# Kernel tuning notes

Measured on AMD Instinct MI355X. Metric: run time of the kernel, lower is better.

## Reference

```python
import jax, jax.numpy as jnp
import numpy as np

EMBED = 256
HEADS = 8
LEVELS = 4
POINTS = 4
HEAD_DIM = EMBED // HEADS
SHAPES = np.array([[100, 134], [50, 67], [25, 34], [13, 17]], dtype=np.int64)  # (H, W) per level


def setup_inputs() -> dict:
    key = jax.random.key(0)
    ks = jax.random.split(key, 11)
    bs = 2
    nv = int(SHAPES.prod(axis=1).sum())  # 17821
    nq = nv
    s = 0.02
    return {
        "query": jax.random.normal(ks[0], (bs, nq, EMBED), jnp.float32),
        "reference_points": jax.random.uniform(ks[1], (bs, nq, LEVELS, 2), jnp.float32),
        "spatial_shapes": jnp.asarray(SHAPES),
        "Wv": jax.random.normal(ks[2], (EMBED, EMBED), jnp.float32) * s,
        "bv": jnp.zeros((EMBED,), jnp.float32),
        "Woff": jax.random.normal(ks[3], (HEADS * LEVELS * POINTS * 2, EMBED), jnp.float32) * s,
        "boff": jax.random.normal(ks[4], (HEADS * LEVELS * POINTS * 2,), jnp.float32) * s,
        "Wattn": jax.random.normal(ks[5], (HEADS * LEVELS * POINTS, EMBED), jnp.float32) * s,
        "battn": jnp.zeros((HEADS * LEVELS * POINTS,), jnp.float32),
        "Wout": jax.random.normal(ks[6], (EMBED, EMBED), jnp.float32) * s,
        "bout": jnp.zeros((EMBED,), jnp.float32),
    }


def _msda(value, shapes, loc, attn):
    # value: [bs, nv, heads, d]; loc: [bs, nq, heads, L, P, 2]; attn: [bs, nq, heads, L, P]
    bs, nq = loc.shape[0], loc.shape[1]
    out = jnp.zeros((bs, nq, HEADS, HEAD_DIM), value.dtype)
    bi = jnp.arange(bs)[:, None, None, None]
    hi = jnp.arange(HEADS)[None, None, :, None]
    start = 0
    for lvl in range(LEVELS):
        H, W = int(shapes[lvl, 0]), int(shapes[lvl, 1])
        v = value[:, start:start + H * W].reshape(bs, H, W, HEADS, HEAD_DIM)
        start += H * W
        l = loc[:, :, :, lvl]                      # [bs, nq, heads, P, 2]
        # grid_sample align_corners=False: x = ((2*loc-1+1)*W - 1)/2 = loc*W - 0.5
        x = l[..., 0] * W - 0.5
        y = l[..., 1] * H - 0.5
        x0 = jnp.floor(x); y0 = jnp.floor(y)
        wx = x - x0; wy = y - y0
        x0i = x0.astype(jnp.int32); y0i = y0.astype(jnp.int32)

        def corner(yi, xi):
            valid = ((yi >= 0) & (yi < H) & (xi >= 0) & (xi < W)).astype(v.dtype)
            vals = v[bi, jnp.clip(yi, 0, H - 1), jnp.clip(xi, 0, W - 1), hi]  # [bs,nq,heads,P,d]
            return vals * valid[..., None]

        samp = (corner(y0i, x0i) * ((1 - wy) * (1 - wx))[..., None]
                + corner(y0i, x0i + 1) * ((1 - wy) * wx)[..., None]
                + corner(y0i + 1, x0i) * (wy * (1 - wx))[..., None]
                + corner(y0i + 1, x0i + 1) * (wy * wx)[..., None])
        out = out + jnp.einsum('bqhpd,bqhp->bqhd', samp, attn[:, :, :, lvl])
    return out.reshape(bs, nq, EMBED)


def reference(query, reference_points, spatial_shapes, Wv, bv, Woff, boff, Wattn, battn, Wout, bout):
    shapes = np.asarray(spatial_shapes)  # concrete per-level (H, W)
    bs, nq, _ = query.shape
    value = (query @ Wv.T + bv).reshape(bs, nq, HEADS, HEAD_DIM)
    off = (query @ Woff.T + boff).reshape(bs, nq, HEADS, LEVELS, POINTS, 2)
    attn = jax.nn.softmax((query @ Wattn.T + battn).reshape(bs, nq, HEADS, LEVELS * POINTS), axis=-1)
    attn = attn.reshape(bs, nq, HEADS, LEVELS, POINTS)
    norm = jnp.stack([jnp.asarray(shapes[:, 1]), jnp.asarray(shapes[:, 0])], -1).astype(query.dtype)  # (W, H)
    loc = reference_points[:, :, None, :, None, :] + off / norm[None, None, None, :, None, :]
    out = _msda(value, shapes, loc, attn)
    out = out @ Wout.T + bout
    return query + out
```

## Files before the change

kernel.cpp:

```cpp
#include <hip/hip_runtime.h>
#include <math.h>

#define M_TOTAL 35642
#define NQ_ 17821
#define NV_ 17821
#define EMB 256
#define KDIM 256
#define QB 8
#define BM 64
#define BN 64
#define NTILES 10
#define MTILES ((M_TOTAL + BM - 1) / BM)

#define WS_VAL_OFF   0ull
#define WS_VAL_BYTES (2ull * M_TOTAL * EMB)
#define WS_OFFW_OFF  (WS_VAL_OFF + WS_VAL_BYTES)
#define WS_OFFW_BYTES (2ull * M_TOTAL * EMB)
#define WS_ATT_OFF   (WS_OFFW_OFF + WS_OFFW_BYTES)
#define WS_ATT_BYTES (2ull * M_TOTAL * 128)
#define WS_SAMP_OFF  (WS_ATT_OFF + WS_ATT_BYTES)
#define WS_SAMP_BYTES (2ull * M_TOTAL * EMB)
#define WS_NEED2     (WS_SAMP_OFF + WS_SAMP_BYTES)
#define WS_WH_OFF    WS_SAMP_OFF

using f16x8 = __attribute__((ext_vector_type(8))) _Float16;
using f32x4 = __attribute__((ext_vector_type(4))) float;
typedef _Float16 h2 __attribute__((ext_vector_type(2)));

__device__ __forceinline__ unsigned short f2h(float f) {
  union { _Float16 h; unsigned short u; } v; v.h = (_Float16)f; return v.u;
}

__device__ __forceinline__ void async_cp16(const void* g, void* l) {
  __builtin_amdgcn_global_load_lds(
      (const __attribute__((address_space(1))) unsigned int*)g,
      (__attribute__((address_space(3))) unsigned int*)l, 16, 0, 0);
}

template <int NWG>
__device__ __forceinline__ int xcd_swz(int bid) {
  constexpr int q8 = NWG >> 3;
  constexpr int r8 = NWG & 7;
  const int xcd = bid & 7, idx = bid >> 3;
  return (xcd < r8 ? xcd * (q8 + 1) : r8 * (q8 + 1) + (xcd - r8) * q8) + idx;
}

__global__ __launch_bounds__(256) void k_prep(
    const float* __restrict__ Wv, const float* __restrict__ Woff,
    const float* __restrict__ Wattn, _Float16* __restrict__ WH) {
  const int i = blockIdx.x * 256 + threadIdx.x;
  if (i >= 640 * 256 / 8) return;
  const int e   = i * 8;
  const int row = e >> 8;
  const int col = e & 255;
  const float* src = (row < 256) ? (Wv + (size_t)row * 256)
                   : (row < 512) ? (Woff + (size_t)(row - 256) * 256)
                                 : (Wattn + (size_t)(row - 512) * 256);
  const float4 a = *reinterpret_cast<const float4*>(src + col);
  const float4 b = *reinterpret_cast<const float4*>(src + col + 4);
  union { _Float16 h[8]; uint4 u; } p;
  p.h[0] = (_Float16)a.x; p.h[1] = (_Float16)a.y; p.h[2] = (_Float16)a.z; p.h[3] = (_Float16)a.w;
  p.h[4] = (_Float16)b.x; p.h[5] = (_Float16)b.y; p.h[6] = (_Float16)b.z; p.h[7] = (_Float16)b.w;
  *reinterpret_cast<uint4*>(WH + e) = p.u;
}

__global__ __launch_bounds__(256) void k_gemm1(
    const float* __restrict__ Q,
    const _Float16* __restrict__ WH,
    const float* __restrict__ bv, const float* __restrict__ boff,
    const float* __restrict__ battn,
    unsigned short* __restrict__ valH,
    unsigned short* __restrict__ offH,
    unsigned short* __restrict__ attH) {

  __shared__ _Float16 Sh[BM * 256];

  const int t = threadIdx.x;
  const int lane = t & 63;
  const int wid = t >> 6;
  const int wr = wid >> 1, wc = wid & 1;
  const int swz = xcd_swz<MTILES * 2>(blockIdx.x);
  const int mt = swz >> 1;
  const int ng = swz & 1;
  const int mb = mt * BM;

#pragma unroll
  for (int i = 0; i < 16; ++i) {
    const int g    = i * 256 + t;
    const int row  = g >> 6;
    const int c4   = g & 63;
    const int c8   = c4 >> 1;
    const int half = c4 & 1;
    const int eo   = row * 256 + ((c8 ^ (row & 7)) * 8) + half * 4;
    int ar = mb + row; if (ar > M_TOTAL - 1) ar = M_TOTAL - 1;
    const float4 qa = *reinterpret_cast<const float4*>(Q + (size_t)ar * KDIM + c4 * 4);
    union { _Float16 h[4]; uint2 u; } p;
    p.h[0] = (_Float16)qa.x; p.h[1] = (_Float16)qa.y;
    p.h[2] = (_Float16)qa.z; p.h[3] = (_Float16)qa.w;
    *reinterpret_cast<uint2*>(&Sh[eo]) = p.u;
  }
  __syncthreads();

  f16x8 af[8][2];
#pragma unroll
  for (int kk = 0; kk < 8; ++kk)
#pragma unroll
    for (int f = 0; f < 2; ++f) {
      const int arow = wr * 32 + f * 16 + (lane & 15);
      const int ac   = (kk * 4 + (lane >> 4)) ^ (arow & 7);
      af[kk][f] = *reinterpret_cast<f16x8*>(&Sh[arow * 256 + ac * 8]);
    }
  __syncthreads();

  for (int nti = 0; nti < 5; ++nti) {
    const int nt = ng * 5 + nti;
    const int nb = nt * BN;
#pragma unroll
    for (int i = 0; i < 8; ++i) {
      const int g   = i * 256 + t;
      const int row = g >> 5;
      const int c8s = (g & 31) ^ (row & 7);
      async_cp16(WH + (size_t)(nb + row) * 256 + c8s * 8,
                 &Sh[(i * 256 + wid * 64) * 8]);
    }
    __syncthreads();

    f32x4 acc[2][2];
#pragma unroll
    for (int a = 0; a < 2; ++a)
#pragma unroll
      for (int b = 0; b < 2; ++b) acc[a][b] = (f32x4)0.f;

#pragma unroll
    for (int kk = 0; kk < 8; ++kk) {
      f16x8 bf[2];
#pragma unroll
      for (int f = 0; f < 2; ++f) {
        const int brow = wc * 32 + f * 16 + (lane & 15);
        const int bc   = (kk * 4 + (lane >> 4)) ^ (brow & 7);
        bf[f] = *reinterpret_cast<f16x8*>(&Sh[brow * 256 + bc * 8]);
      }
#pragma unroll
      for (int fr = 0; fr < 2; ++fr)
#pragma unroll
        for (int fc = 0; fc < 2; ++fc)
          acc[fr][fc] = __builtin_amdgcn_mfma_f32_16x16x32_f16(af[kk][fr], bf[fc], acc[fr][fc], 0, 0, 0);
    }
    __syncthreads();

    {
      const float* bsec; int nsb;
      if (nt < 4)      { bsec = bv;    nsb = 0;   }
      else if (nt < 8) { bsec = boff;  nsb = 256; }
      else             { bsec = battn; nsb = 512; }
      const int nrow0 = nb - nsb;
      const int col = lane & 15;
      const int rg4 = lane >> 4;
      float bias2[2];
      bias2[0] = bsec[nrow0 + wc * 32 + 0 * 16 + col];
      bias2[1] = bsec[nrow0 + wc * 32 + 1 * 16 + col];
      unsigned short* Ep = reinterpret_cast<unsigned short*>(Sh);
#pragma unroll
      for (int fr = 0; fr < 2; ++fr)
#pragma unroll
        for (int fc = 0; fc < 2; ++fc)
#pragma unroll
          for (int j = 0; j < 4; ++j)
            Ep[(wr * 32 + fr * 16 + rg4 * 4 + j) * 64 + wc * 32 + fc * 16 + col] =
                f2h(acc[fr][fc][j] + bias2[fc]);
      __syncthreads();

#pragma unroll
      for (int i = 0; i < 2; ++i) {
        const int g   = i * 256 + t;
        const int row = g >> 3;
        const int ch  = g & 7;
        const int m   = mb + row;
        if (m < M_TOTAL) {
          const uint4 v = *reinterpret_cast<const uint4*>(&Ep[row * 64 + ch * 8]);
          const int n0 = nb + ch * 8;
          if (nsb == 0) {
            const int b  = (m >= NQ_) ? 1 : 0;
            const int mm = m - b * NQ_;
            *reinterpret_cast<uint4*>(&valH[((size_t)(b * 8 + (n0 >> 5)) * NV_ + mm) * 32 + (n0 & 31)]) = v;
          } else if (nsb == 256) {
            *reinterpret_cast<uint4*>(&offH[(size_t)m * 256 + (n0 - 256)]) = v;
          } else {
            *reinterpret_cast<uint4*>(&attH[(size_t)m * 128 + (n0 - 512)]) = v;
          }
        }
      }
    }
    __syncthreads();
  }
}

__global__ __launch_bounds__(256) void k_gather(
    const float* __restrict__ refp,
    const unsigned short* __restrict__ valH,
    const unsigned short* __restrict__ offH,
    const unsigned short* __restrict__ attH,
    unsigned short* __restrict__ sampH) {

  const int t  = threadIdx.x;
  const int q0 = xcd_swz<(M_TOTAL + QB - 1) / QB>(blockIdx.x) * QB;
  const int q  = t >> 5;
  const int h  = (t >> 2) & 7;
  const int dq = t & 3;
  const int m  = q0 + q;
  const int mc = min(m, M_TOTAL - 1);

  float aw[16];
  {
    const f16x8 a0 = *reinterpret_cast<const f16x8*>(attH + (size_t)mc * 128 + h * 16);
    const f16x8 a1 = *reinterpret_cast<const f16x8*>(attH + (size_t)mc * 128 + h * 16 + 8);
#pragma unroll
    for (int i = 0; i < 8; ++i) { aw[i] = (float)a0[i]; aw[8 + i] = (float)a1[i]; }
  }
  float mx = aw[0];
#pragma unroll
  for (int i = 1; i < 16; ++i) mx = fmaxf(mx, aw[i]);
  float ssum = 0.f;
#pragma unroll
  for (int i = 0; i < 16; ++i) { aw[i] = __expf(aw[i] - mx); ssum += aw[i]; }
  const float inv = 1.0f / ssum;
#pragma unroll
  for (int i = 0; i < 16; ++i) aw[i] *= inv;

  h2 sacc2[4];
#pragma unroll
  for (int j = 0; j < 4; ++j) { sacc2[j][0] = (_Float16)0.f; sacc2[j][1] = (_Float16)0.f; }

  {
    constexpr int LH[4] = {100, 50, 25, 13};
    constexpr int LW[4] = {134, 67, 34, 17};
    constexpr int LS[4] = {0, 13400, 16750, 17600};
    const int b = (mc >= NQ_) ? 1 : 0;
    const float* rp = refp + (size_t)mc * 8;
    const uint4* vb = reinterpret_cast<const uint4*>(valH) + (size_t)(b * 8 + h) * NV_ * 4 + dq;

#pragma unroll
    for (int lvl = 0; lvl < 4; ++lvl) {
      const int Hl = LH[lvl], Wl = LW[lvl], st = LS[lvl];
      const float Hf = (float)Hl, Wf = (float)Wl;
      const float2 rxy = *reinterpret_cast<const float2*>(rp + lvl * 2);
      const f16x8 ov = *reinterpret_cast<const f16x8*>(offH + (size_t)mc * 256 + h * 32 + lvl * 8);
#pragma unroll
      for (int pp = 0; pp < 2; ++pp) {
        h2 wq[2][4];
        size_t idx[2][4];
#pragma unroll
        for (int s = 0; s < 2; ++s) {
          const int p = pp * 2 + s;
          const float ox = (float)ov[p * 2 + 0];
          const float oy = (float)ov[p * 2 + 1];
          const float x = fmaf(rxy.x, Wf, ox) - 0.5f;
          const float y = fmaf(rxy.y, Hf, oy) - 0.5f;
          const float xf = floorf(x), yf = floorf(y);
          const float wx = x - xf, wy = y - yf;
          const int x0i = (int)xf, y0i = (int)yf;
          const int x1i = x0i + 1, y1i = y0i + 1;
          const float vx0 = (x0i >= 0 && x0i < Wl) ? 1.f : 0.f;
          const float vx1 = (x1i >= 0 && x1i < Wl) ? 1.f : 0.f;
          const float vy0 = (y0i >= 0 && y0i < Hl) ? 1.f : 0.f;
          const float vy1 = (y1i >= 0 && y1i < Hl) ? 1.f : 0.f;
          const int x0c = min(max(x0i, 0), Wl - 1);
          const int x1c = min(max(x1i, 0), Wl - 1);
          const int y0c = min(max(y0i, 0), Hl - 1);
          const int y1c = min(max(y1i, 0), Hl - 1);
          const float a = aw[lvl * 4 + p];
          const float w00 = a * (1.f - wy) * (1.f - wx) * (vy0 * vx0);
          const float w01 = a * (1.f - wy) * wx         * (vy0 * vx1);
          const float w10 = a * wy         * (1.f - wx) * (vy1 * vx0);
          const float w11 = a * wy         * wx         * (vy1 * vx1);
          const _Float16 h00 = (_Float16)w00, h01 = (_Float16)w01;
          const _Float16 h10 = (_Float16)w10, h11 = (_Float16)w11;
          wq[s][0] = h2{h00, h00};
          wq[s][1] = h2{h01, h01};
          wq[s][2] = h2{h10, h10};
          wq[s][3] = h2{h11, h11};
          idx[s][0] = (size_t)(st + y0c * Wl + x0c) * 4;
          idx[s][1] = (size_t)(st + y0c * Wl + x1c) * 4;
          idx[s][2] = (size_t)(st + y1c * Wl + x0c) * 4;
          idx[s][3] = (size_t)(st + y1c * Wl + x1c) * 4;
        }
        union UV { uint4 u; h2 hh[4]; };
        UV c[2][4];
#pragma unroll
        for (int s = 0; s < 2; ++s)
#pragma unroll
          for (int k = 0; k < 4; ++k) c[s][k].u = vb[idx[s][k]];
#pragma unroll
        for (int s = 0; s < 2; ++s)
#pragma unroll
          for (int k = 0; k < 4; ++k)
#pragma unroll
            for (int j = 0; j < 4; ++j)
              sacc2[j] += c[s][k].hh[j] * wq[s][k];
        __builtin_amdgcn_sched_group_barrier(0x002, 96, 0);
        __builtin_amdgcn_sched_group_barrier(0x020, 8, 0);
        __builtin_amdgcn_sched_group_barrier(0x002, 64, 0);
      }
    }
  }

  if (m < M_TOTAL) {
    union { h2 hh[4]; uint4 u; } pk;
#pragma unroll
    for (int j = 0; j < 4; ++j) pk.hh[j] = sacc2[j];
    *reinterpret_cast<uint4*>(sampH + (size_t)m * 256 + h * 32 + dq * 8) = pk.u;
  }
}

__global__ __launch_bounds__(256) void k_gemm2(
    const float* __restrict__ Q,
    const unsigned short* __restrict__ sampH,
    const float* __restrict__ Wout, const float* __restrict__ bout,
    float* __restrict__ out) {

  __shared__ _Float16 As[BM * 128];
  __shared__ _Float16 Bs[BN * 128];

  const int swz = xcd_swz<MTILES * 4>(blockIdx.x);
  const int nt = swz & 3;
  const int mt = swz >> 2;
  const int t = threadIdx.x;
  const int lane = t & 63;
  const int wid = t >> 6;
  const int wr = wid >> 1, wc = wid & 1;
  const int mb = mt * BM;
  const int nb = nt * BN;

  f32x4 acc[2][2];
#pragma unroll
  for (int a = 0; a < 2; ++a)
#pragma unroll
    for (int b = 0; b < 2; ++b) acc[a][b] = (f32x4)0.f;

  for (int kc = 0; kc < 2; ++kc) {
    const int koff = kc * 128;
#pragma unroll
    for (int i = 0; i < 4; ++i) {
      const int g   = i * 256 + t;
      const int row = g >> 4;
      const int c8s = (g & 15) ^ (row & 7);
      int ar = mb + row; if (ar > M_TOTAL - 1) ar = M_TOTAL - 1;
      async_cp16(sampH + (size_t)ar * 256 + koff + c8s * 8,
                 &As[(i * 256 + wid * 64) * 8]);
    }
#pragma unroll
    for (int i = 0; i < 4; ++i) {
      const int g   = i * 256 + t;
      const int row = g >> 4;
      const int c8  = g & 15;
      const int eo  = row * 128 + (c8 ^ (row & 7)) * 8;
      const float4 w0 = *reinterpret_cast<const float4*>(Wout + (size_t)(nb + row) * KDIM + koff + c8 * 8);
      const float4 w1 = *reinterpret_cast<const float4*>(Wout + (size_t)(nb + row) * KDIM + koff + c8 * 8 + 4);
      union { _Float16 h[8]; uint4 u; } pb;
      pb.h[0] = (_Float16)w0.x; pb.h[1] = (_Float16)w0.y;
      pb.h[2] = (_Float16)w0.z; pb.h[3] = (_Float16)w0.w;
      pb.h[4] = (_Float16)w1.x; pb.h[5] = (_Float16)w1.y;
      pb.h[6] = (_Float16)w1.z; pb.h[7] = (_Float16)w1.w;
      *reinterpret_cast<uint4*>(&Bs[eo]) = pb.u;
    }
    __syncthreads();

#pragma unroll
    for (int kk = 0; kk < 4; ++kk) {
      f16x8 af[2], bf[2];
#pragma unroll
      for (int f = 0; f < 2; ++f) {
        const int arow = wr * 32 + f * 16 + (lane & 15);
        const int ac   = (kk * 4 + (lane >> 4)) ^ (arow & 7);
        af[f] = *reinterpret_cast<f16x8*>(&As[arow * 128 + ac * 8]);
        const int brow = wc * 32 + f * 16 + (lane & 15);
        const int bc   = (kk * 4 + (lane >> 4)) ^ (brow & 7);
        bf[f] = *reinterpret_cast<f16x8*>(&Bs[brow * 128 + bc * 8]);
      }
#pragma unroll
      for (int fr = 0; fr < 2; ++fr)
#pragma unroll
        for (int fc = 0; fc < 2; ++fc)
          acc[fr][fc] = __builtin_amdgcn_mfma_f32_16x16x32_f16(af[fr], bf[fc], acc[fr][fc], 0, 0, 0);
    }
    __syncthreads();
  }

  {
    const int col = lane & 15;
    const int rg4 = lane >> 4;
    float bias2[2];
    bias2[0] = bout[nb + wc * 32 + 0 * 16 + col];
    bias2[1] = bout[nb + wc * 32 + 1 * 16 + col];
    float* Ep = reinterpret_cast<float*>(As);
#pragma unroll
    for (int fr = 0; fr < 2; ++fr)
#pragma unroll
      for (int fc = 0; fc < 2; ++fc)
#pragma unroll
        for (int j = 0; j < 4; ++j)
          Ep[(wr * 32 + fr * 16 + rg4 * 4 + j) * 64 + wc * 32 + fc * 16 + col] =
              acc[fr][fc][j] + bias2[fc];
    __syncthreads();

#pragma unroll
    for (int i = 0; i < 4; ++i) {
      const int g   = i * 256 + t;
      const int row = g >> 4;
      const int ch  = g & 15;
      const int m   = mb + row;
      if (m < M_TOTAL) {
        const int n0 = nb + ch * 4;
        float4 v = *reinterpret_cast<const float4*>(&Ep[row * 64 + ch * 4]);
        const float4 q4 = *reinterpret_cast<const float4*>(Q + (size_t)m * EMB + n0);
        v.x += q4.x; v.y += q4.y; v.z += q4.z; v.w += q4.w;
        *reinterpret_cast<float4*>(out + (size_t)m * EMB + n0) = v;
      }
    }
  }
}

extern "C" void kernel_launch(void* const* d_in, const int* in_sizes, int n_in,
                              void* d_out, int out_size, void* d_ws, size_t ws_size,
                              hipStream_t stream) {
  const float* Q     = (const float*)d_in[0];
  const float* refp  = (const float*)d_in[1];
  const float* Wv    = (const float*)d_in[3];
  const float* bv    = (const float*)d_in[4];
  const float* Woff  = (const float*)d_in[5];
  const float* boff  = (const float*)d_in[6];
  const float* Wattn = (const float*)d_in[7];
  const float* battn = (const float*)d_in[8];
  const float* Wout  = (const float*)d_in[9];
  const float* bout  = (const float*)d_in[10];
  float* out = (float*)d_out;

  if (ws_size < WS_NEED2) return;

  unsigned short* valH  = (unsigned short*)((char*)d_ws + WS_VAL_OFF);
  unsigned short* offH  = (unsigned short*)((char*)d_ws + WS_OFFW_OFF);
  unsigned short* attH  = (unsigned short*)((char*)d_ws + WS_ATT_OFF);
  unsigned short* sampH = (unsigned short*)((char*)d_ws + WS_SAMP_OFF);
  _Float16*       WH    = (_Float16*)((char*)d_ws + WS_WH_OFF);

  const int nblk_q8 = (M_TOTAL + QB - 1) / QB;

  k_prep<<<dim3(80), dim3(256), 0, stream>>>(Wv, Woff, Wattn, WH);
  k_gemm1<<<dim3(MTILES * 2), dim3(256), 0, stream>>>(Q, WH, bv, boff, battn,
                                                      valH, offH, attH);
  k_gather<<<dim3(nblk_q8), dim3(256), 0, stream>>>(refp, valH, offH, attH, sampH);
  k_gemm2<<<dim3(MTILES * 4), dim3(256), 0, stream>>>(Q, sampH, Wout, bout, out);
}
```

Baseline: 135.4 us.

## Split B-tile staging into K halves to overlap loads with MFMA

The projection GEMM now stages each 64-row weight tile in two K halves. The second half's async copy is issued before the MFMAs on the first half, so part of the global-load latency is hidden behind compute. The epilogue staging buffer moves into the second-half region, which removes the trailing barrier per N-tile. The cost is an extra barrier between the halves, plus correctness now depends on the barrier placement keeping the epilogue region from being overwritten while it is still read.

```diff
diff --git a/kernel.cpp b/kernel.cpp
--- a/kernel.cpp
+++ b/kernel.cpp
@@ -112,18 +112,25 @@
     }
   __syncthreads();
 
+#define STAGE_B_HALF(kh)                                                      \
+  do {                                                                        \
+    _Pragma("unroll")                                                         \
+    for (int i = 0; i < 4; ++i) {                                             \
+      const int g   = i * 256 + t;                                            \
+      const int row = g >> 4;                                                 \
+      const int c8s = (kh) * 16 + ((g & 15) ^ (row & 7));                     \
+      async_cp16(WH + (size_t)(nb + row) * 256 + c8s * 8,                     \
+                 &Sh[(kh) * 8192 + (i * 256 + wid * 64) * 8]);                \
+    }                                                                         \
+  } while (0)
+
   for (int nti = 0; nti < 5; ++nti) {
     const int nt = ng * 5 + nti;
     const int nb = nt * BN;
-#pragma unroll
-    for (int i = 0; i < 8; ++i) {
-      const int g   = i * 256 + t;
-      const int row = g >> 5;
-      const int c8s = (g & 31) ^ (row & 7);
-      async_cp16(WH + (size_t)(nb + row) * 256 + c8s * 8,
-                 &Sh[(i * 256 + wid * 64) * 8]);
-    }
-    __syncthreads();
+
+    STAGE_B_HALF(0);
+    __syncthreads();
+    STAGE_B_HALF(1);
 
     f32x4 acc[2][2];
 #pragma unroll
@@ -132,13 +139,30 @@
       for (int b = 0; b < 2; ++b) acc[a][b] = (f32x4)0.f;
 
 #pragma unroll
-    for (int kk = 0; kk < 8; ++kk) {
+    for (int kk = 0; kk < 4; ++kk) {
       f16x8 bf[2];
 #pragma unroll
       for (int f = 0; f < 2; ++f) {
         const int brow = wc * 32 + f * 16 + (lane & 15);
         const int bc   = (kk * 4 + (lane >> 4)) ^ (brow & 7);
-        bf[f] = *reinterpret_cast<f16x8*>(&Sh[brow * 256 + bc * 8]);
+        bf[f] = *reinterpret_cast<f16x8*>(&Sh[brow * 128 + bc * 8]);
+      }
+#pragma unroll
+      for (int fr = 0; fr < 2; ++fr)
+#pragma unroll
+        for (int fc = 0; fc < 2; ++fc)
+          acc[fr][fc] = __builtin_amdgcn_mfma_f32_16x16x32_f16(af[kk][fr], bf[fc], acc[fr][fc], 0, 0, 0);
+    }
+    __syncthreads();
+
+#pragma unroll
+    for (int kk = 4; kk < 8; ++kk) {
+      f16x8 bf[2];
+#pragma unroll
+      for (int f = 0; f < 2; ++f) {
+        const int brow = wc * 32 + f * 16 + (lane & 15);
+        const int bc   = ((kk - 4) * 4 + (lane >> 4)) ^ (brow & 7);
+        bf[f] = *reinterpret_cast<f16x8*>(&Sh[8192 + brow * 128 + bc * 8]);
       }
 #pragma unroll
       for (int fr = 0; fr < 2; ++fr)
@@ -159,7 +183,7 @@
       float bias2[2];
       bias2[0] = bsec[nrow0 + wc * 32 + 0 * 16 + col];
       bias2[1] = bsec[nrow0 + wc * 32 + 1 * 16 + col];
-      unsigned short* Ep = reinterpret_cast<unsigned short*>(Sh);
+      unsigned short* Ep = reinterpret_cast<unsigned short*>(&Sh[8192]);
 #pragma unroll
       for (int fr = 0; fr < 2; ++fr)
 #pragma unroll
@@ -191,8 +215,8 @@
         }
       }
     }
-    __syncthreads();
-  }
+  }
+#undef STAGE_B_HALF
 }
 
 __global__ __launch_bounds__(256) void k_gather(
```

After: 135.8 us. Within noise of the previous version (+0.3%).
